# Performance work log

Measured on AMD Instinct MI355X. Metric: run time of the kernel, lower is better.

Reference implementation:

```python
import jax, jax.numpy as jnp
import numpy as np

K = 3          # kernel_size
EPS = 1e-5     # BatchNorm eps


def setup_inputs() -> dict:
    key = jax.random.key(0)
    k1, k2, k3 = jax.random.split(key, 3)
    n, C, H, W = 8, 64, 128, 128
    x = jax.random.normal(k1, (n, C, H, W), dtype=jnp.float32)
    conv_w = jax.random.normal(k2, (C * K * K, C), dtype=jnp.float32) * np.sqrt(2.0 / (C * K * K))
    bn_gamma = jnp.ones((C * K * K,), dtype=jnp.float32)
    bn_beta = jnp.zeros((C * K * K,), dtype=jnp.float32)
    bn_mean = jnp.zeros((C * K * K,), dtype=jnp.float32)
    bn_var = jax.random.uniform(k3, (C * K * K,), dtype=jnp.float32)
    return {"x": x, "conv_w": conv_w, "bn_gamma": bn_gamma, "bn_beta": bn_beta,
            "bn_mean": bn_mean, "bn_var": bn_var}


def reference(x, conv_w, bn_gamma, bn_beta, bn_mean, bn_var):
    n, C, H, W = x.shape
    # ---- per-image dynamic filter: GAP -> 1x1 conv -> BN (eval) -> softmax over k^2 ----
    f = x.mean(axis=(2, 3))                       # (n, C)
    f = f @ conv_w.T                              # (n, C*9)  (1x1 conv on 1x1 map, no bias)
    f = (f - bn_mean) * (bn_gamma / jnp.sqrt(bn_var + EPS)) + bn_beta
    f = jax.nn.softmax(f.reshape(n, C, K * K), axis=-1)   # softmax over kernel positions
    # ---- reflect-pad + unfold (im2col), row-major kernel offsets matching F.unfold ----
    xp = jnp.pad(x, ((0, 0), (0, 0), (1, 1), (1, 1)), mode="reflect")
    patches = jnp.stack([xp[:, :, i:i + H, j:j + W]
                         for i in range(K) for j in range(K)], axis=2)  # (n, C, 9, H, W)
    # ---- softmax-weighted dynamic sum over the 9 taps ----
    out = jnp.einsum("nckhw,nck->nchw", patches, f)
    return out, x - out
```

## Files before the change

### kernel.cpp

```cpp
#include <hip/hip_runtime.h>

#define WW 128
#define HWSZ 16384
#define CC 64
#define NPLANE 512
#define NCHW 8388608
#define BN_EPS 1e-5f

__global__ __launch_bounds__(256) void dc_mean_kernel(const float* __restrict__ x,
                                                      float* __restrict__ means) {
    const int plane = blockIdx.x;
    const float4* xp = (const float4*)(x + (size_t)plane * HWSZ);
    float s = 0.f;
#pragma unroll
    for (int i = 0; i < 16; ++i) {
        float4 v = xp[threadIdx.x + i * 256];
        s += v.x + v.y + v.z + v.w;
    }
    for (int off = 32; off > 0; off >>= 1)
        s += __shfl_down(s, off, 64);
    __shared__ float wsum[4];
    if ((threadIdx.x & 63) == 0) wsum[threadIdx.x >> 6] = s;
    __syncthreads();
    if (threadIdx.x == 0)
        means[plane] = (wsum[0] + wsum[1] + wsum[2] + wsum[3]) * (1.0f / 16384.0f);
}

__global__ __launch_bounds__(256) void dc_conv_kernel(const float* __restrict__ x,
                                                      const float* __restrict__ means,
                                                      const float* __restrict__ conv_w,
                                                      const float* __restrict__ gamma,
                                                      const float* __restrict__ beta,
                                                      const float* __restrict__ bn_mean,
                                                      const float* __restrict__ bn_var,
                                                      float* __restrict__ out) {
    const int plane = blockIdx.x >> 2;
    const int band  = blockIdx.x & 3;
    const int tid   = threadIdx.x;
    const int n = plane >> 6;
    const int c = plane & 63;

    __shared__ float lv[9];
    if (tid < 144) {
        const int j    = tid >> 4;
        const int part = tid & 15;
        const int jj = c * 9 + j;
        float4 mv = *(const float4*)(means + n * CC + part * 4);
        float4 wv = *(const float4*)(conv_w + (size_t)jj * CC + part * 4);
        float d = mv.x * wv.x + mv.y * wv.y + mv.z * wv.z + mv.w * wv.w;
        d += __shfl_down(d, 8, 16);
        d += __shfl_down(d, 4, 16);
        d += __shfl_down(d, 2, 16);
        d += __shfl_down(d, 1, 16);
        if (part == 0) {
            const float g = gamma[jj] * rsqrtf(bn_var[jj] + BN_EPS);
            lv[j] = (d - bn_mean[jj]) * g + beta[jj];
        }
    }
    __syncthreads();

    float w9[9];
    {
        float m = lv[0];
#pragma unroll
        for (int t = 1; t < 9; ++t) m = fmaxf(m, lv[t]);
        float den = 0.f;
        float e[9];
#pragma unroll
        for (int t = 0; t < 9; ++t) { e[t] = __expf(lv[t] - m); den += e[t]; }
        const float inv = 1.0f / den;
#pragma unroll
        for (int t = 0; t < 9; ++t) w9[t] = e[t] * inv;
    }

    const int r  = tid >> 5;
    const int q  = tid & 31;
    const int w0 = q * 4;
    const float* xpl = x + (size_t)plane * HWSZ;

#pragma unroll
    for (int it = 0; it < 4; ++it) {
        const int h  = band * 32 + it * 8 + r;
        const int hm = (h == 0)   ? 1   : h - 1;
        const int hp = (h == 127) ? 126 : h + 1;
        const int rows[3] = {hm, h, hp};

        float V[3][6];
#pragma unroll
        for (int ri = 0; ri < 3; ++ri) {
            const float* rowp = xpl + rows[ri] * WW;
            float4 c4 = *(const float4*)(rowp + w0);
            V[ri][1] = c4.x; V[ri][2] = c4.y; V[ri][3] = c4.z; V[ri][4] = c4.w;
            V[ri][0] = (w0 == 0)   ? c4.y : rowp[w0 - 1];
            V[ri][5] = (w0 == 124) ? c4.z : rowp[w0 + 4];
        }

        float o[4];
#pragma unroll
        for (int p = 0; p < 4; ++p) {
            float acc = 0.f;
#pragma unroll
            for (int ri = 0; ri < 3; ++ri)
#pragma unroll
                for (int t = 0; t < 3; ++t)
                    acc = fmaf(w9[ri * 3 + t], V[ri][p + t], acc);
            o[p] = acc;
        }

        const size_t base = (size_t)plane * HWSZ + (size_t)h * WW + w0;
        float4 ov = {o[0], o[1], o[2], o[3]};
        *(float4*)(out + base) = ov;
        float4 dv = {V[1][1] - o[0], V[1][2] - o[1], V[1][3] - o[2], V[1][4] - o[3]};
        *(float4*)(out + NCHW + base) = dv;
    }
}

extern "C" void kernel_launch(void* const* d_in, const int* in_sizes, int n_in,
                              void* d_out, int out_size, void* d_ws, size_t ws_size,
                              hipStream_t stream) {
    const float* x       = (const float*)d_in[0];
    const float* conv_w  = (const float*)d_in[1];
    const float* gamma   = (const float*)d_in[2];
    const float* beta    = (const float*)d_in[3];
    const float* bn_mean = (const float*)d_in[4];
    const float* bn_var  = (const float*)d_in[5];
    float* out = (float*)d_out;
    float* means = (float*)d_ws;

    dc_mean_kernel<<<NPLANE, 256, 0, stream>>>(x, means);
    dc_conv_kernel<<<NPLANE * 4, 256, 0, stream>>>(x, means, conv_w, gamma, beta,
                                                   bn_mean, bn_var, out);
}
```

Baseline: 113.7 us.

## Stream rows through registers with sliding window and shuffle-based halos

Each thread now walks 8 consecutive rows and keeps a 3-row register window, loading one new row per output row instead of three. Horizontal halo values come from neighbouring lanes via shuffles instead of extra scalar global loads. Blocks cover half a plane rather than a quarter, so the grid is halved, and outputs are written with nontemporal stores. This cuts redundant global and L2 reads, at the cost of fewer blocks and some extra per-thread serial latency.

After: 108.3 us. 4.8% less time.

```diff
diff --git a/kernel.cpp b/kernel.cpp
--- a/kernel.cpp
+++ b/kernel.cpp
@@ -7,14 +7,16 @@
 #define NCHW 8388608
 #define BN_EPS 1e-5f
 
+typedef float v4f __attribute__((ext_vector_type(4)));
+
 __global__ __launch_bounds__(256) void dc_mean_kernel(const float* __restrict__ x,
                                                       float* __restrict__ means) {
     const int plane = blockIdx.x;
-    const float4* xp = (const float4*)(x + (size_t)plane * HWSZ);
+    const v4f* xp = (const v4f*)(x + (size_t)plane * HWSZ);
     float s = 0.f;
 #pragma unroll
     for (int i = 0; i < 16; ++i) {
-        float4 v = xp[threadIdx.x + i * 256];
+        v4f v = xp[threadIdx.x + i * 256];
         s += v.x + v.y + v.z + v.w;
     }
     for (int off = 32; off > 0; off >>= 1)
@@ -34,8 +36,8 @@
                                                       const float* __restrict__ bn_mean,
                                                       const float* __restrict__ bn_var,
                                                       float* __restrict__ out) {
-    const int plane = blockIdx.x >> 2;
-    const int band  = blockIdx.x & 3;
+    const int plane = blockIdx.x >> 1;
+    const int band  = blockIdx.x & 1;
     const int tid   = threadIdx.x;
     const int n = plane >> 6;
     const int c = plane & 63;
@@ -45,8 +47,8 @@
         const int j    = tid >> 4;
         const int part = tid & 15;
         const int jj = c * 9 + j;
-        float4 mv = *(const float4*)(means + n * CC + part * 4);
-        float4 wv = *(const float4*)(conv_w + (size_t)jj * CC + part * 4);
+        v4f mv = *(const v4f*)(means + n * CC + part * 4);
+        v4f wv = *(const v4f*)(conv_w + (size_t)jj * CC + part * 4);
         float d = mv.x * wv.x + mv.y * wv.y + mv.z * wv.z + mv.w * wv.w;
         d += __shfl_down(d, 8, 16);
         d += __shfl_down(d, 4, 16);
@@ -73,46 +75,62 @@
         for (int t = 0; t < 9; ++t) w9[t] = e[t] * inv;
     }
 
-    const int r  = tid >> 5;
+    const int g  = tid >> 5;
     const int q  = tid & 31;
     const int w0 = q * 4;
+    const int r0 = band * 64 + g * 8;
     const float* xpl = x + (size_t)plane * HWSZ;
 
+    v4f cP, cC, cN, cX;
+    float eP0, eP1, eC0, eC1, eN0, eN1, eX0, eX1;
+
+#define LOADROW(R, c4, e0, e1)                                              \
+    {                                                                       \
+        int RR = ((R) < 0) ? 1 : (((R) > 127) ? 126 : (R));                 \
+        c4 = *(const v4f*)(xpl + RR * WW + w0);                             \
+        float lft = __shfl_up(c4.w, 1, 32);                                 \
+        float rgt = __shfl_down(c4.x, 1, 32);                               \
+        e0 = (w0 == 0)   ? c4.y : lft;           \
+        e1 = (w0 == 124) ? c4.z : rgt;          \
+    }
+
+    LOADROW(r0 - 1, cP, eP0, eP1);
+    LOADROW(r0,     cC, eC0, eC1);
+    LOADROW(r0 + 1, cN, eN0, eN1);
+
 #pragma unroll
-    for (int it = 0; it < 4; ++it) {
-        const int h  = band * 32 + it * 8 + r;
-        const int hm = (h == 0)   ? 1   : h - 1;
-        const int hp = (h == 127) ? 126 : h + 1;
-        const int rows[3] = {hm, h, hp};
+    for (int i = 0; i < 8; ++i) {
+        const int h = r0 + i;
+        if (i < 7) { LOADROW(h + 2, cX, eX0, eX1); }
 
-        float V[3][6];
-#pragma unroll
-        for (int ri = 0; ri < 3; ++ri) {
-            const float* rowp = xpl + rows[ri] * WW;
-            float4 c4 = *(const float4*)(rowp + w0);
-            V[ri][1] = c4.x; V[ri][2] = c4.y; V[ri][3] = c4.z; V[ri][4] = c4.w;
-            V[ri][0] = (w0 == 0)   ? c4.y : rowp[w0 - 1];
-            V[ri][5] = (w0 == 124) ? c4.z : rowp[w0 + 4];
-        }
+        const float VP[6] = {eP0, cP.x, cP.y, cP.z, cP.w, eP1};
+        const float VC[6] = {eC0, cC.x, cC.y, cC.z, cC.w, eC1};
+        const float VN[6] = {eN0, cN.x, cN.y, cN.z, cN.w, eN1};
 
         float o[4];
 #pragma unroll
         for (int p = 0; p < 4; ++p) {
             float acc = 0.f;
 #pragma unroll
-            for (int ri = 0; ri < 3; ++ri)
-#pragma unroll
-                for (int t = 0; t < 3; ++t)
-                    acc = fmaf(w9[ri * 3 + t], V[ri][p + t], acc);
+            for (int t = 0; t < 3; ++t) {
+                acc = fmaf(w9[t],     VP[p + t], acc);
+                acc = fmaf(w9[3 + t], VC[p + t], acc);
+                acc = fmaf(w9[6 + t], VN[p + t], acc);
+            }
             o[p] = acc;
         }
 
         const size_t base = (size_t)plane * HWSZ + (size_t)h * WW + w0;
-        float4 ov = {o[0], o[1], o[2], o[3]};
-        *(float4*)(out + base) = ov;
-        float4 dv = {V[1][1] - o[0], V[1][2] - o[1], V[1][3] - o[2], V[1][4] - o[3]};
-        *(float4*)(out + NCHW + base) = dv;
+        v4f ov = {o[0], o[1], o[2], o[3]};
+        v4f dv = {cC.x - o[0], cC.y - o[1], cC.z - o[2], cC.w - o[3]};
+        __builtin_nontemporal_store(ov, (v4f*)(out + base));
+        __builtin_nontemporal_store(dv, (v4f*)(out + NCHW + base));
+
+        cP = cC; eP0 = eC0; eP1 = eC1;
+        cC = cN; eC0 = eN0; eC1 = eN1;
+        cN = cX; eN0 = eX0; eN1 = eX1;
     }
+#undef LOADROW
 }
 
 extern "C" void kernel_launch(void* const* d_in, const int* in_sizes, int n_in,
@@ -128,6 +146,6 @@
     float* means = (float*)d_ws;
 
     dc_mean_kernel<<<NPLANE, 256, 0, stream>>>(x, means);
-    dc_conv_kernel<<<NPLANE * 4, 256, 0, stream>>>(x, means, conv_w, gamma, beta,
+    dc_conv_kernel<<<NPLANE * 2, 256, 0, stream>>>(x, means, conv_w, gamma, beta,
                                                    bn_mean, bn_var, out);
 }
```
